# Optimization experiments

Measured on AMD Instinct MI355X. Metric: run time of the kernel, lower is better.

Reference implementation:

```python
import jax, jax.numpy as jnp
import numpy as np
import math

B, T, D = 2, 2048, 1024
N_EXP, TOP_K = 8, 2
CAP_FACTOR = 1.25  # train_capacity (module in training mode)
MIN_CAP = 4


def _capacity(num_tokens):
    cap = math.floor(TOP_K * CAP_FACTOR * num_tokens / N_EXP)
    cap += cap % 2
    return max(cap, MIN_CAP)


def setup_inputs() -> dict:
    key = jax.random.key(0)
    k1, k2 = jax.random.split(key)
    x = jax.random.normal(k1, (B, T, D), dtype=jnp.float32)
    w_g = jax.random.normal(k2, (N_EXP, D), dtype=jnp.float32) * 0.02
    return {"x": x, "w_g": w_g}


def reference(x, w_g):
    Bx, Tx, Dx = x.shape
    n_tok = Bx * Tx
    cap = _capacity(n_tok)  # static: depends only on shapes

    # router runs in full precision (router_use_full_prec=True)
    logits = jnp.einsum('btd,ed->bte', x.astype(jnp.float32), w_g.astype(jnp.float32))
    logits = logits.reshape(n_tok, N_EXP)

    top_v, top_i = jax.lax.top_k(logits, TOP_K)          # [n_tok, k]
    # softmax over (-inf)-masked logits == softmax over the k selected logits
    probs_k = jax.nn.softmax(top_v, axis=-1)             # [n_tok, k]

    # expert one-hot mask, ordered [k, tokens, n_exp] (matches torch permute)
    exp_mask = jax.nn.one_hot(top_i, N_EXP, dtype=jnp.int32)   # [n_tok, k, n_exp]
    exp_mask = jnp.transpose(exp_mask, (1, 0, 2))              # [k, n_tok, n_exp]

    # position-in-expert-queue rank via cumsum over flattened (k*tokens)
    rank = jnp.cumsum(exp_mask.reshape(TOP_K * n_tok, N_EXP), axis=0) - 1
    rank = rank.reshape(TOP_K, n_tok, N_EXP)

    exp_mask = exp_mask * (rank < cap).astype(jnp.int32)       # drop overflow tokens
    used_capacity = jnp.sum(exp_mask, axis=(0, 1))             # [n_exp]

    rank_sel = jnp.sum(exp_mask * rank, axis=-1)               # [k, n_tok] int
    keep = jnp.sum(exp_mask, axis=-1).astype(jnp.float32)      # [k, n_tok] 0/1
    w_sel = probs_k.T * keep                                   # [k, n_tok]

    # combine weights: scatter instead of the O(k*tok*n_exp*cap) outer product
    cb_weight = jnp.zeros((n_tok, N_EXP, cap), dtype=jnp.float32)
    tok_ids = jnp.arange(n_tok)
    for k in range(TOP_K):  # tiny static loop over top_k
        cb_weight = cb_weight.at[tok_ids, top_i[:, k], rank_sel[k]].add(w_sel[k])

    sec_mask = cb_weight != 0
    return used_capacity, cb_weight, sec_mask
```

## Files before the change

### kernel.cpp

```cpp
#include <hip/hip_runtime.h>

#define N_TOK   4096
#define DDIM    1024
#define N_EXP   8
#define CAP     1280
#define ROW     (N_EXP * CAP)
#define CB_ELEMS (N_TOK * ROW)
#define OUT_FLOATS (8 + 2 * (size_t)CB_ELEMS)

typedef __attribute__((ext_vector_type(4))) float f32x4;


__global__ __launch_bounds__(256) void router_kernel(
    const float* __restrict__ x, const float* __restrict__ wg,
    unsigned int* __restrict__ pk,
    float* __restrict__ p0, float* __restrict__ p1)
{
    __shared__ int se0[4], se1[4];
    const int wave = threadIdx.x >> 6;
    const int lane = threadIdx.x & 63;
    const int t = blockIdx.x * 4 + wave;

    const float4* xt  = (const float4*)(x + (size_t)t * DDIM);
    const float4* wg4 = (const float4*)wg;

    float acc[N_EXP];
#pragma unroll
    for (int e = 0; e < N_EXP; ++e) acc[e] = 0.f;

#pragma unroll
    for (int it = 0; it < 4; ++it) {
        const int d4 = lane + it * 64;
        const float4 xv = xt[d4];
#pragma unroll
        for (int e = 0; e < N_EXP; ++e) {
            const float4 wv = wg4[e * 256 + d4];
            acc[e] = fmaf(xv.x, wv.x,
                     fmaf(xv.y, wv.y,
                     fmaf(xv.z, wv.z,
                     fmaf(xv.w, wv.w, acc[e]))));
        }
    }

#pragma unroll
    for (int e = 0; e < N_EXP; ++e) {
#pragma unroll
        for (int off = 32; off >= 1; off >>= 1)
            acc[e] += __shfl_xor(acc[e], off, 64);
    }

    if (lane == 0) {
        float v0 = -3.402823466e38f, v1 = -3.402823466e38f;
        int   i0 = 0, i1 = 0;
#pragma unroll
        for (int e = 0; e < N_EXP; ++e) {
            const float v = acc[e];
            if (v > v0)      { v1 = v0; i1 = i0; v0 = v; i0 = e; }
            else if (v > v1) { v1 = v;  i1 = e; }
        }
        const float ex  = expf(v1 - v0);
        const float inv = 1.f / (1.f + ex);
        p0[t] = inv;
        p1[t] = ex * inv;
        se0[wave] = i0;
        se1[wave] = i1;
    }
    __syncthreads();

    if (threadIdx.x == 0) {
        const int b = blockIdx.x;
        unsigned short* pks = (unsigned short*)pk;
        const unsigned short h0 = (unsigned short)(se0[0] | (se0[1] << 4) |
                                                   (se0[2] << 8) | (se0[3] << 12));
        const unsigned short h1 = (unsigned short)(se1[0] | (se1[1] << 4) |
                                                   (se1[2] << 8) | (se1[3] << 12));
        pks[b]        = h0;
        pks[1024 + b] = h1;
    }
}

__global__ __launch_bounds__(256) void fixup_kernel(
    const unsigned int* __restrict__ pk, const float* __restrict__ p0,
    const float* __restrict__ p1, float* __restrict__ out)
{
    __shared__ unsigned int spk[1024];
#pragma unroll
    for (int j = 0; j < 4; ++j)
        spk[threadIdx.x + j * 256] = pk[threadIdx.x + j * 256];
    __syncthreads();

    const int wave = threadIdx.x >> 6;
    const int lane = threadIdx.x & 63;
    const int i    = blockIdx.x * 4 + wave;
    const int t    = i & (N_TOK - 1);
    const int k    = i >> 12;

    unsigned int w[16];
#pragma unroll
    for (int j = 0; j < 16; ++j) w[j] = spk[lane + j * 64];

    const int e = (int)((spk[i >> 3] >> ((i & 7) * 4)) & 0xF);
    int cnt = 0;
#pragma unroll
    for (int j = 0; j < 16; ++j) {
        const int bi = (lane + j * 64) * 8;
#pragma unroll
        for (int s = 0; s < 8; ++s)
            cnt += (bi + s < i && (int)((w[j] >> (4 * s)) & 0xF) == e) ? 1 : 0;
    }
#pragma unroll
    for (int off = 32; off >= 1; off >>= 1)
        cnt += __shfl_xor(cnt, off, 64);

    if (lane == 0 && cnt < CAP) {
        const float wv = k ? p1[t] : p0[t];
        float* cb = out + 8 + (size_t)t * ROW + (size_t)e * CAP + cnt;
        cb[0]        = wv;
        cb[CB_ELEMS] = (wv != 0.f) ? 1.f : 0.f;
    }

    if (blockIdx.x == 0) {
#pragma unroll
        for (int q = 0; q < 2; ++q) {
            const int ee = wave * 2 + q;
            int c = 0;
#pragma unroll
            for (int j = 0; j < 16; ++j) {
#pragma unroll
                for (int s = 0; s < 8; ++s)
                    c += ((int)((w[j] >> (4 * s)) & 0xF) == ee) ? 1 : 0;
            }
#pragma unroll
            for (int off = 32; off >= 1; off >>= 1)
                c += __shfl_xor(c, off, 64);
            if (lane == 0) out[ee] = (float)min(c, CAP);
        }
    }
}

extern "C" void kernel_launch(void* const* d_in, const int* in_sizes, int n_in,
                              void* d_out, int out_size, void* d_ws, size_t ws_size,
                              hipStream_t stream)
{
    const float* x  = (const float*)d_in[0];
    const float* wg = (const float*)d_in[1];
    float* out = (float*)d_out;

    char*         ws = (char*)d_ws;
    unsigned int* pk = (unsigned int*)(ws);
    float*        p0 = (float*)(ws + 4096);
    float*        p1 = (float*)(ws + 20480);

    router_kernel<<<N_TOK / 4, 256, 0, stream>>>(x, wg, pk, p0, p1);

    hipMemsetAsync(d_out, 0, OUT_FLOATS * sizeof(float), stream);

    fixup_kernel<<<2048, 256, 0, stream>>>(pk, p0, p1, out);
}
```

Before: 79.84 us.

## Fuse output zero-fill into router kernel and store experts as bytes

Drops the separate hipMemsetAsync over the whole combine-weight and mask output. The router kernel now runs one block per token and zeroes that token's slice of the output with 16-byte vector stores while computing the gating logits. Expert indices are stored as one byte per token instead of packed 4-bit nibbles, and the fixup kernel scans twice as many words to match. The intent is to save a launch and overlap the bandwidth-bound zero-fill with the router compute, at the cost of a router kernel that now does far more memory traffic.

```diff
diff --git a/kernel.cpp b/kernel.cpp
--- a/kernel.cpp
+++ b/kernel.cpp
@@ -6,55 +6,56 @@
 #define CAP     1280
 #define ROW     (N_EXP * CAP)
 #define CB_ELEMS (N_TOK * ROW)
-#define OUT_FLOATS (8 + 2 * (size_t)CB_ELEMS)
 
 typedef __attribute__((ext_vector_type(4))) float f32x4;
 
 
-__global__ __launch_bounds__(256) void router_kernel(
+__global__ __launch_bounds__(256) void router_zero_kernel(
     const float* __restrict__ x, const float* __restrict__ wg,
-    unsigned int* __restrict__ pk,
-    float* __restrict__ p0, float* __restrict__ p1)
+    unsigned char* __restrict__ eb,
+    float* __restrict__ p0, float* __restrict__ p1,
+    float* __restrict__ out)
 {
-    __shared__ int se0[4], se1[4];
+    __shared__ float part[4][N_EXP];
+    const int t    = blockIdx.x;
     const int wave = threadIdx.x >> 6;
     const int lane = threadIdx.x & 63;
-    const int t = blockIdx.x * 4 + wave;
+    const int d4   = wave * 64 + lane;
 
-    const float4* xt  = (const float4*)(x + (size_t)t * DDIM);
-    const float4* wg4 = (const float4*)wg;
+    const float4 xv = ((const float4*)(x + (size_t)t * DDIM))[d4];
+    float4 wv[N_EXP];
+#pragma unroll
+    for (int e = 0; e < N_EXP; ++e)
+        wv[e] = ((const float4*)wg)[e * 256 + d4];
+
+    f32x4* b4 = (f32x4*)(out + 8 + (size_t)t * (2 * ROW));
+    const f32x4 z = {0.f, 0.f, 0.f, 0.f};
+#pragma unroll
+    for (int it = 0; it < 20; ++it)
+        b4[threadIdx.x + it * 256] = z;
 
     float acc[N_EXP];
 #pragma unroll
-    for (int e = 0; e < N_EXP; ++e) acc[e] = 0.f;
-
-#pragma unroll
-    for (int it = 0; it < 4; ++it) {
-        const int d4 = lane + it * 64;
-        const float4 xv = xt[d4];
-#pragma unroll
-        for (int e = 0; e < N_EXP; ++e) {
-            const float4 wv = wg4[e * 256 + d4];
-            acc[e] = fmaf(xv.x, wv.x,
-                     fmaf(xv.y, wv.y,
-                     fmaf(xv.z, wv.z,
-                     fmaf(xv.w, wv.w, acc[e]))));
-        }
-    }
-
-#pragma unroll
     for (int e = 0; e < N_EXP; ++e) {
+        acc[e] = fmaf(xv.x, wv[e].x,
+                 fmaf(xv.y, wv[e].y,
+                 fmaf(xv.z, wv[e].z, xv.w * wv[e].w)));
 #pragma unroll
         for (int off = 32; off >= 1; off >>= 1)
             acc[e] += __shfl_xor(acc[e], off, 64);
     }
+    if (lane == 0) {
+#pragma unroll
+        for (int e = 0; e < N_EXP; ++e) part[wave][e] = acc[e];
+    }
+    __syncthreads();
 
-    if (lane == 0) {
+    if (threadIdx.x == 0) {
         float v0 = -3.402823466e38f, v1 = -3.402823466e38f;
         int   i0 = 0, i1 = 0;
 #pragma unroll
         for (int e = 0; e < N_EXP; ++e) {
-            const float v = acc[e];
+            const float v = part[0][e] + part[1][e] + part[2][e] + part[3][e];
             if (v > v0)      { v1 = v0; i1 = i0; v0 = v; i0 = e; }
             else if (v > v1) { v1 = v;  i1 = e; }
         }
@@ -62,31 +63,19 @@
         const float inv = 1.f / (1.f + ex);
         p0[t] = inv;
         p1[t] = ex * inv;
-        se0[wave] = i0;
-        se1[wave] = i1;
-    }
-    __syncthreads();
-
-    if (threadIdx.x == 0) {
-        const int b = blockIdx.x;
-        unsigned short* pks = (unsigned short*)pk;
-        const unsigned short h0 = (unsigned short)(se0[0] | (se0[1] << 4) |
-                                                   (se0[2] << 8) | (se0[3] << 12));
-        const unsigned short h1 = (unsigned short)(se1[0] | (se1[1] << 4) |
-                                                   (se1[2] << 8) | (se1[3] << 12));
-        pks[b]        = h0;
-        pks[1024 + b] = h1;
+        eb[t]         = (unsigned char)i0;
+        eb[N_TOK + t] = (unsigned char)i1;
     }
 }
 
 __global__ __launch_bounds__(256) void fixup_kernel(
-    const unsigned int* __restrict__ pk, const float* __restrict__ p0,
+    const unsigned int* __restrict__ eb32, const float* __restrict__ p0,
     const float* __restrict__ p1, float* __restrict__ out)
 {
-    __shared__ unsigned int spk[1024];
+    __shared__ unsigned int spk[2048];
 #pragma unroll
-    for (int j = 0; j < 4; ++j)
-        spk[threadIdx.x + j * 256] = pk[threadIdx.x + j * 256];
+    for (int j = 0; j < 8; ++j)
+        spk[threadIdx.x + j * 256] = eb32[threadIdx.x + j * 256];
     __syncthreads();
 
     const int wave = threadIdx.x >> 6;
@@ -95,18 +84,18 @@
     const int t    = i & (N_TOK - 1);
     const int k    = i >> 12;
 
-    unsigned int w[16];
+    unsigned int w[32];
 #pragma unroll
-    for (int j = 0; j < 16; ++j) w[j] = spk[lane + j * 64];
+    for (int j = 0; j < 32; ++j) w[j] = spk[lane + j * 64];
 
-    const int e = (int)((spk[i >> 3] >> ((i & 7) * 4)) & 0xF);
+    const int e = (int)((spk[i >> 2] >> ((i & 3) * 8)) & 0xFF);
     int cnt = 0;
 #pragma unroll
-    for (int j = 0; j < 16; ++j) {
-        const int bi = (lane + j * 64) * 8;
+    for (int j = 0; j < 32; ++j) {
+        const int bi = (lane + j * 64) * 4;
 #pragma unroll
-        for (int s = 0; s < 8; ++s)
-            cnt += (bi + s < i && (int)((w[j] >> (4 * s)) & 0xF) == e) ? 1 : 0;
+        for (int s = 0; s < 4; ++s)
+            cnt += (bi + s < i && (int)((w[j] >> (8 * s)) & 0xFF) == e) ? 1 : 0;
     }
 #pragma unroll
     for (int off = 32; off >= 1; off >>= 1)
@@ -125,10 +114,10 @@
             const int ee = wave * 2 + q;
             int c = 0;
 #pragma unroll
-            for (int j = 0; j < 16; ++j) {
+            for (int j = 0; j < 32; ++j) {
 #pragma unroll
-                for (int s = 0; s < 8; ++s)
-                    c += ((int)((w[j] >> (4 * s)) & 0xF) == ee) ? 1 : 0;
+                for (int s = 0; s < 4; ++s)
+                    c += ((int)((w[j] >> (8 * s)) & 0xFF) == ee) ? 1 : 0;
             }
 #pragma unroll
             for (int off = 32; off >= 1; off >>= 1)
@@ -146,14 +135,11 @@
     const float* wg = (const float*)d_in[1];
     float* out = (float*)d_out;
 
-    char*         ws = (char*)d_ws;
-    unsigned int* pk = (unsigned int*)(ws);
-    float*        p0 = (float*)(ws + 4096);
-    float*        p1 = (float*)(ws + 20480);
+    char*          ws = (char*)d_ws;
+    unsigned char* eb = (unsigned char*)(ws);
+    float*         p0 = (float*)(ws + 8192);
+    float*         p1 = (float*)(ws + 24576);
 
-    router_kernel<<<N_TOK / 4, 256, 0, stream>>>(x, wg, pk, p0, p1);
-
-    hipMemsetAsync(d_out, 0, OUT_FLOATS * sizeof(float), stream);
-
-    fixup_kernel<<<2048, 256, 0, stream>>>(pk, p0, p1, out);
+    router_zero_kernel<<<N_TOK, 256, 0, stream>>>(x, wg, eb, p0, p1, out);
+    fixup_kernel<<<2048, 256, 0, stream>>>((const unsigned int*)eb, p0, p1, out);
 }
```

New measurement: 87.97 us. 1.1x slower.
